# Kernel tuning notes

Measured on AMD Instinct MI355X. Metric: run time of the kernel, lower is better.

Reference implementation:

```python
import jax, jax.numpy as jnp
import numpy as np

N = 50000
E = 1600000
IN, HID, OUT = 32, 64, 64

def setup_inputs() -> dict:
    key = jax.random.key(0)
    ks = jax.random.split(key, 10)
    x1 = jax.random.normal(ks[0], (N, IN), dtype=jnp.float32)
    x2 = jax.random.normal(ks[1], (N, IN), dtype=jnp.float32)
    ei1 = jax.random.randint(ks[2], (2, E), 0, N, dtype=jnp.int64)
    ei2 = jax.random.randint(ks[3], (2, E), 0, N, dtype=jnp.int64)
    s1 = 1.0 / np.sqrt(2 * IN)
    s2 = 1.0 / np.sqrt(2 * HID)
    W1 = jax.random.uniform(ks[4], (2 * IN, HID), jnp.float32, -s1, s1)
    b1 = jax.random.uniform(ks[5], (HID,), jnp.float32, -s1, s1)
    prelu_a = jnp.full((HID,), 0.25, dtype=jnp.float32)  # PReLU per-channel init
    W2 = jax.random.uniform(ks[6], (2 * HID, OUT), jnp.float32, -s2, s2)
    b2 = jax.random.uniform(ks[7], (OUT,), jnp.float32, -s2, s2)
    return {"x1": x1, "edge_index1": ei1, "x2": x2, "edge_index2": ei2,
            "W1": W1, "b1": b1, "prelu_a": prelu_a, "W2": W2, "b2": b2}

def _edge_conv(x, src, dst, W, b, n_nodes):
    # PyG EdgeConv: msg = MLP([x_i, x_j - x_i]), aggr = max over incoming edges
    xi = x[dst]                     # [E, d] target node feats
    xj = x[src]                     # [E, d] source node feats
    msg = jax.nn.relu(jnp.concatenate([xi, xj - xi], axis=-1) @ W + b)  # [E, out]
    agg = jax.ops.segment_max(msg, dst, num_segments=n_nodes)
    return jnp.where(jnp.isfinite(agg), agg, 0.0)  # nodes with no in-edges -> 0

def _prelu(x, a):
    return jnp.where(x >= 0, x, a * x)

def _embed(x, edge_index, W1, b1, prelu_a, W2, b2):
    src, dst = edge_index[0], edge_index[1]
    h = _prelu(_edge_conv(x, src, dst, W1, b1, x.shape[0]), prelu_a)
    return _edge_conv(h, src, dst, W2, b2, x.shape[0])

def reference(x1, edge_index1, x2, edge_index2, W1, b1, prelu_a, W2, b2):
    e1 = _embed(x1, edge_index1, W1, b1, prelu_a, W2, b2)
    e2 = _embed(x2, edge_index2, W1, b1, prelu_a, W2, b2)
    return (e1, e2)
```

## Files before the change

### kernel.cpp

```cpp
#include <hip/hip_runtime.h>
#include <hip/hip_fp16.h>


constexpr int HID   = 64;
constexpr int TILE  = 128;
constexpr int TSH   = 7;
constexpr int HTILE = 64;
constexpr int CAP   = 5120;
constexpr int MAXNB = 512;
constexpr int EPT   = 8;
constexpr int CAPN  = 96;

typedef _Float16 half8 __attribute__((ext_vector_type(8)));
typedef float    f32x4 __attribute__((ext_vector_type(4)));

__device__ __forceinline__ unsigned int pkmax(unsigned int a, unsigned int b) {
    unsigned int d;
    asm("v_pk_max_f16 %0, %1, %2" : "=v"(d) : "v"(a), "v"(b));
    return d;
}
__device__ __forceinline__ unsigned int f2hbits(float f) {
    const __half h = __float2half_rn(f);
    return (unsigned int)*reinterpret_cast<const unsigned short*>(&h);
}
__device__ __forceinline__ float h2f(unsigned int b16) {
    const unsigned short b = (unsigned short)b16;
    __half h;
    *reinterpret_cast<unsigned short*>(&h) = b;
    return __half2float(h);
}

struct G {
    const float* x;
    const int*   src;
    const int*   dst;
    int* bcnt;
    unsigned int* bin;
    float*          u;
    unsigned short* vk;
    float*          out;
};

__global__ __launch_bounds__(256) void prep_w_kernel(
    const float* __restrict__ W1, const float* __restrict__ W2,
    _Float16* __restrict__ Wc1, _Float16* __restrict__ Wc2,
    unsigned short* __restrict__ vkS0, unsigned short* __restrict__ vkS1, int N)
{
    const int i = blockIdx.x * 256 + threadIdx.x;
    if (i < 32 * 64) {
        const int k = i >> 6, c = i & 63;
        const float lo = W1[k * 64 + c], hi = W1[(32 + k) * 64 + c];
        Wc1[k * 128 + c]      = (_Float16)(lo - hi);
        Wc1[k * 128 + 64 + c] = (_Float16)hi;
    }
    const int j = i - 32 * 64;
    if (j >= 0 && j < 64 * 64) {
        const int k = j >> 6, c = j & 63;
        const float lo = W2[k * 64 + c], hi = W2[(64 + k) * 64 + c];
        Wc2[k * 128 + c]      = (_Float16)(lo - hi);
        Wc2[k * 128 + 64 + c] = (_Float16)hi;
    }
    const int q = i - (32 * 64 + 64 * 64);
    if (q >= 0 && q < 2 * HID) {
        if (q < HID) vkS0[(size_t)N * HID + q]       = 0xFC00u;
        else         vkS1[(size_t)N * HID + (q-HID)] = 0xFC00u;
    }
}

__global__ __launch_bounds__(256) void bin_kernel(G g0, G g1, int E, int NB) {
    const G g = blockIdx.y ? g1 : g0;
    __shared__ int lh[MAXNB];
    __shared__ int lb[MAXNB];
    for (int i = threadIdx.x; i < NB; i += 256) lh[i] = 0;
    __syncthreads();

    const int base = blockIdx.x * 256 * EPT;
    unsigned int rec[EPT];
    int bb[EPT];
    #pragma unroll
    for (int k = 0; k < EPT; ++k) {
        const int i = base + k * 256 + threadIdx.x;
        if (i < E) {
            const int d = g.dst[i];
            const int s = g.src[i];
            rec[k] = ((unsigned int)s << TSH) | (unsigned int)(d & (TILE - 1));
            bb[k]  = d >> TSH;
            atomicAdd(&lh[bb[k]], 1);
        } else bb[k] = -1;
    }
    __syncthreads();
    for (int t = threadIdx.x; t < NB; t += 256) {
        const int c = lh[t];
        lb[t] = c ? atomicAdd(&g.bcnt[t], c) : 0;
        lh[t] = 0;
    }
    __syncthreads();
    #pragma unroll
    for (int k = 0; k < EPT; ++k) {
        if (bb[k] >= 0) {
            const int off = atomicAdd(&lh[bb[k]], 1);
            const int pos = lb[bb[k]] + off;
            if (pos < CAP)
                g.bin[(size_t)bb[k] * CAP + pos] = rec[k];
        }
    }
}

template<int K>
__global__ __launch_bounds__(256) void gemm_mfma_kernel(
    G g0, G g1, const _Float16* __restrict__ Wc,
    const float* __restrict__ bias, int N)
{
    const G g = blockIdx.y ? g1 : g0;
    constexpr int KH = K / 32;
    const int lane = threadIdx.x & 63;
    const int m    = lane & 15;
    const int quad = lane >> 4;
    const int wid  = (blockIdx.x * 256 + threadIdx.x) >> 6;
    const int nW   = (gridDim.x * 256) >> 6;

    half8 bf[8][KH];
    #pragma unroll
    for (int t = 0; t < 8; ++t)
        #pragma unroll
        for (int h = 0; h < KH; ++h)
            #pragma unroll
            for (int j = 0; j < 8; ++j)
                bf[t][h][j] = Wc[(h * 32 + quad * 8 + j) * 128 + t * 16 + m];

    float bv[4];
    #pragma unroll
    for (int t = 0; t < 4; ++t) bv[t] = bias[t * 16 + m];

    const float* __restrict__ inp = (K == 32) ? g.x : g.out;
    const int tiles = (N + 15) / 16;

    for (int tile = wid; tile < tiles; tile += nW) {
        const int nbase = tile * 16;
        const int nodeA = min(nbase + m, N - 1);
        const float4* rp = (const float4*)(inp + (size_t)nodeA * K);

        half8 a[KH];
        #pragma unroll
        for (int h = 0; h < KH; ++h) {
            const float4 f0 = rp[h * 8 + quad * 2];
            const float4 f1 = rp[h * 8 + quad * 2 + 1];
            a[h][0] = (_Float16)f0.x; a[h][1] = (_Float16)f0.y;
            a[h][2] = (_Float16)f0.z; a[h][3] = (_Float16)f0.w;
            a[h][4] = (_Float16)f1.x; a[h][5] = (_Float16)f1.y;
            a[h][6] = (_Float16)f1.z; a[h][7] = (_Float16)f1.w;
        }

        f32x4 acc[8];
        #pragma unroll
        for (int t = 0; t < 8; ++t) {
            acc[t] = (f32x4){0.f, 0.f, 0.f, 0.f};
            #pragma unroll
            for (int h = 0; h < KH; ++h)
                acc[t] = __builtin_amdgcn_mfma_f32_16x16x32_f16(
                    a[h], bf[t][h], acc[t], 0, 0, 0);
        }

        #pragma unroll
        for (int r = 0; r < 4; ++r) {
            const int node = nbase + quad * 4 + r;
            if (node < N) {
                float* urow = g.u + (size_t)node * HID;
                #pragma unroll
                for (int t = 0; t < 4; ++t)
                    urow[t * 16 + m] = acc[t][r] + bv[t];
                const unsigned int e0 = f2hbits(acc[4][r]);
                const unsigned int e1 = f2hbits(acc[5][r]);
                const unsigned int e2 = f2hbits(acc[6][r]);
                const unsigned int e3 = f2hbits(acc[7][r]);
                uint2 pack;
                pack.x = (e1 << 16) | e0;
                pack.y = (e3 << 16) | e2;
                ((uint2*)(g.vk + (size_t)node * HID))[m] = pack;
            }
        }
    }
}

__global__ __launch_bounds__(256) void agg_kernel(G g0, G g1, int N, int NB, int two) {
    int idx, gi;
    if (two) {
        const int bid = blockIdx.x;
        const int xcd = bid & 7;
        gi  = xcd >> 2;
        idx = (bid >> 3) * 4 + (xcd & 3);
    } else { gi = 0; idx = blockIdx.x; }
    if (idx >= 2 * NB) return;
    const int b    = idx >> 1;
    const int half = idx & 1;
    const G g = gi ? g1 : g0;

    __shared__ int lcnt[HTILE];
    __shared__ unsigned short lrec[HTILE][CAPN];
    for (int i = threadIdx.x; i < HTILE; i += 256) lcnt[i] = 0;
    __syncthreads();

    const int cnt  = min(g.bcnt[b], CAP);
    const int hsel = half << 6;
    const unsigned int* __restrict__ bp = g.bin + (size_t)b * CAP;
    for (int i = threadIdx.x; i < cnt; i += 256) {
        const unsigned int rec = bp[i];
        const int d = rec & (TILE - 1);
        if ((d & 64) == hsel) {
            const int p = atomicAdd(&lcnt[d & 63], 1);
            if (p < CAPN) lrec[d & 63][p] = (unsigned short)(rec >> TSH);
        }
    }
    __syncthreads();
    for (int t = threadIdx.x; t < HTILE; t += 256) {
        const int c  = min(lcnt[t], CAPN);
        const int cp = (c + 7) & ~7;
        for (int p = c; p < cp; ++p) lrec[t][p] = (unsigned short)N;
        lcnt[t] = cp;
    }
    __syncthreads();

    const int grp = threadIdx.x >> 4;
    const int sub = threadIdx.x & 15;
    const uint2* __restrict__ vk2 = (const uint2*)g.vk;

    #pragma unroll
    for (int i = 0; i < 4; ++i) {
        const int nl = grp + 16 * i;
        const int n  = b * TILE + half * HTILE + nl;
        if (n >= N) continue;
        const int cp = lcnt[nl];

        unsigned int m0 = 0xFC00FC00u, m1 = 0xFC00FC00u;
        for (int j = 0; j < cp; j += 8) {
            const uint4 rq = *(const uint4*)(&lrec[nl][j]);
            unsigned int s[8];
            s[0] = rq.x & 0xFFFFu; s[1] = rq.x >> 16;
            s[2] = rq.y & 0xFFFFu; s[3] = rq.y >> 16;
            s[4] = rq.z & 0xFFFFu; s[5] = rq.z >> 16;
            s[6] = rq.w & 0xFFFFu; s[7] = rq.w >> 16;
            uint2 a[8];
            #pragma unroll
            for (int k = 0; k < 8; ++k) a[k] = vk2[(size_t)s[k] * 16 + sub];
            #pragma unroll
            for (int k = 0; k < 8; ++k) {
                m0 = pkmax(m0, a[k].x);
                m1 = pkmax(m1, a[k].y);
            }
        }

        float mv[4];
        mv[0] = h2f(m0 & 0xFFFFu); mv[1] = h2f(m0 >> 16);
        mv[2] = h2f(m1 & 0xFFFFu); mv[3] = h2f(m1 >> 16);

        const bool has = cp > 0;
        const float* __restrict__ urow = g.u + (size_t)n * HID;
        float* __restrict__ orow = g.out + (size_t)n * HID;
        #pragma unroll
        for (int t = 0; t < 4; ++t)
            orow[sub + 16 * t] =
                has ? fmaxf(urow[sub + 16 * t] + mv[t], 0.f) : 0.f;
    }
}


extern "C" void kernel_launch(void* const* d_in, const int* in_sizes, int n_in,
                              void* d_out, int out_size, void* d_ws, size_t ws_size,
                              hipStream_t stream) {
    const float* x1  = (const float*)d_in[0];
    const int*   ei1 = (const int*)d_in[1];
    const float* x2  = (const float*)d_in[2];
    const int*   ei2 = (const int*)d_in[3];
    const float* W1  = (const float*)d_in[4];
    const float* b1  = (const float*)d_in[5];
    const float* W2  = (const float*)d_in[7];
    const float* b2  = (const float*)d_in[8];

    const int N  = in_sizes[0] / 32;
    const int E  = in_sizes[1] / 2;
    const int NB = (N + TILE - 1) / TILE;
    float* out = (float*)d_out;

    const size_t rowB = (size_t)N * HID * sizeof(float);
    const size_t vkB  = ((size_t)(N + 1) * HID * 2 + 63) & ~(size_t)63;
    const size_t binB = ((size_t)NB * CAP * sizeof(int) + 63) & ~(size_t)63;
    const size_t nbB  = ((size_t)(NB + 2) * sizeof(int) + 63) & ~(size_t)63;
    const size_t wc1B = ((size_t)32 * 128 * 2 + 63) & ~(size_t)63;
    const size_t wc2B = ((size_t)64 * 128 * 2 + 63) & ~(size_t)63;

    const int bBlk = (E + 256 * EPT - 1) / (256 * EPT);
    const int gBlk = 512;
    const int pBlk = (32 * 64 + 64 * 64 + 2 * HID + 255) / 256;
    const int aggBlk2 = ((2 * NB + 3) / 4) * 8;
    const int aggBlk1 = 2 * NB;

    _Float16* wc1 = nullptr;
    _Float16* wc2 = nullptr;

    auto run = [&](G ga, G gb, int ny) {
        hipMemsetAsync(ga.bcnt, 0, (size_t)ny * nbB, stream);
        bin_kernel <<<dim3(bBlk, ny), 256, 0, stream>>>(ga, gb, E, NB);
        gemm_mfma_kernel<32><<<dim3(gBlk, ny), 256, 0, stream>>>(ga, gb, wc1, b1, N);
        if (ny == 2) agg_kernel<<<aggBlk2, 256, 0, stream>>>(ga, gb, N, NB, 1);
        else         agg_kernel<<<aggBlk1, 256, 0, stream>>>(ga, ga, N, NB, 0);
        gemm_mfma_kernel<64><<<dim3(gBlk, ny), 256, 0, stream>>>(ga, gb, wc2, b2, N);
        if (ny == 2) agg_kernel<<<aggBlk2, 256, 0, stream>>>(ga, gb, N, NB, 1);
        else         agg_kernel<<<aggBlk1, 256, 0, stream>>>(ga, ga, N, NB, 0);
    };

    char* ws = (char*)d_ws;
    const size_t needBoth = 2 * rowB + 2 * vkB + 2 * binB + 2 * nbB + wc1B + wc2B;

    if (ws_size >= needBoth) {
        float* u0 = (float*)ws;                  ws += rowB;
        float* u1 = (float*)ws;                  ws += rowB;
        unsigned int* bin0 = (unsigned int*)ws;  ws += binB;
        unsigned int* bin1 = (unsigned int*)ws;  ws += binB;
        unsigned short* vk0 = (unsigned short*)ws;  ws += vkB;
        unsigned short* vk1 = (unsigned short*)ws;  ws += vkB;
        wc1 = (_Float16*)ws;                     ws += wc1B;
        wc2 = (_Float16*)ws;                     ws += wc2B;
        int* bcnt0 = (int*)ws;                   ws += nbB;
        int* bcnt1 = (int*)ws;

        G g0{x1, ei1, ei1 + E, bcnt0, bin0, u0, vk0, out};
        G g1{x2, ei2, ei2 + E, bcnt1, bin1, u1, vk1, out + (size_t)N * HID};
        prep_w_kernel<<<pBlk, 256, 0, stream>>>(W1, W2, wc1, wc2, vk0, vk1, N);
        run(g0, g1, 2);
    } else {
        float* u = (float*)ws;                   ws += rowB;
        unsigned int* bin = (unsigned int*)ws;   ws += binB;
        unsigned short* vk = (unsigned short*)ws;  ws += vkB;
        wc1 = (_Float16*)ws;                     ws += wc1B;
        wc2 = (_Float16*)ws;                     ws += wc2B;
        int* bcnt = (int*)ws;

        prep_w_kernel<<<pBlk, 256, 0, stream>>>(W1, W2, wc1, wc2, vk, vk, N);
        for (int g = 0; g < 2; ++g) {
            const int* ei = g ? ei2 : ei1;
            G gp{g ? x2 : x1, ei, ei + E, bcnt, bin,
                 u, vk, out + (size_t)g * N * HID};
            run(gp, gp, 1);
        }
    }
}
```

Before: 264.3 us.

## Split aggregation by feature half instead of node half, relayout vk rows

Each aggregation block now covers all 128 destination nodes of a bin but only half of the 64 feature channels, instead of half the nodes with all channels. The vk row layout is changed so each feature half sits in a contiguous 64-byte span, and each gather loads one 32-bit word per edge rather than a uint2. The aim is for each block to touch half the vk bytes per gathered row, which can improve L2 locality when paired with the XCD-based block mapping. In exchange, every block reads and bins the whole bin record list, and the shared memory for lrec doubles.

```diff
diff --git a/kernel.cpp b/kernel.cpp
--- a/kernel.cpp
+++ b/kernel.cpp
@@ -5,7 +5,6 @@
 constexpr int HID   = 64;
 constexpr int TILE  = 128;
 constexpr int TSH   = 7;
-constexpr int HTILE = 64;
 constexpr int CAP   = 5120;
 constexpr int MAXNB = 512;
 constexpr int EPT   = 8;
@@ -173,46 +172,41 @@
                 const unsigned int e1 = f2hbits(acc[5][r]);
                 const unsigned int e2 = f2hbits(acc[6][r]);
                 const unsigned int e3 = f2hbits(acc[7][r]);
-                uint2 pack;
-                pack.x = (e1 << 16) | e0;
-                pack.y = (e3 << 16) | e2;
-                ((uint2*)(g.vk + (size_t)node * HID))[m] = pack;
+                unsigned int* vr = (unsigned int*)(g.vk + (size_t)node * HID);
+                vr[m]      = (e1 << 16) | e0;
+                vr[16 + m] = (e3 << 16) | e2;
             }
         }
     }
 }
 
 __global__ __launch_bounds__(256) void agg_kernel(G g0, G g1, int N, int NB, int two) {
-    int idx, gi;
+    int b, h, gi;
     if (two) {
         const int bid = blockIdx.x;
         const int xcd = bid & 7;
-        gi  = xcd >> 2;
-        idx = (bid >> 3) * 4 + (xcd & 3);
-    } else { gi = 0; idx = blockIdx.x; }
-    if (idx >= 2 * NB) return;
-    const int b    = idx >> 1;
-    const int half = idx & 1;
+        gi = xcd >> 2;
+        h  = (xcd >> 1) & 1;
+        b  = (bid >> 3) * 2 + (xcd & 1);
+    } else { gi = 0; h = blockIdx.x & 1; b = blockIdx.x >> 1; }
+    if (b >= NB) return;
     const G g = gi ? g1 : g0;
 
-    __shared__ int lcnt[HTILE];
-    __shared__ unsigned short lrec[HTILE][CAPN];
-    for (int i = threadIdx.x; i < HTILE; i += 256) lcnt[i] = 0;
-    __syncthreads();
-
-    const int cnt  = min(g.bcnt[b], CAP);
-    const int hsel = half << 6;
+    __shared__ int lcnt[TILE];
+    __shared__ unsigned short lrec[TILE][CAPN];
+    for (int i = threadIdx.x; i < TILE; i += 256) lcnt[i] = 0;
+    __syncthreads();
+
+    const int cnt = min(g.bcnt[b], CAP);
     const unsigned int* __restrict__ bp = g.bin + (size_t)b * CAP;
     for (int i = threadIdx.x; i < cnt; i += 256) {
         const unsigned int rec = bp[i];
         const int d = rec & (TILE - 1);
-        if ((d & 64) == hsel) {
-            const int p = atomicAdd(&lcnt[d & 63], 1);
-            if (p < CAPN) lrec[d & 63][p] = (unsigned short)(rec >> TSH);
-        }
-    }
-    __syncthreads();
-    for (int t = threadIdx.x; t < HTILE; t += 256) {
+        const int p = atomicAdd(&lcnt[d], 1);
+        if (p < CAPN) lrec[d][p] = (unsigned short)(rec >> TSH);
+    }
+    __syncthreads();
+    for (int t = threadIdx.x; t < TILE; t += 256) {
         const int c  = min(lcnt[t], CAPN);
         const int cp = (c + 7) & ~7;
         for (int p = c; p < cp; ++p) lrec[t][p] = (unsigned short)N;
@@ -220,18 +214,19 @@
     }
     __syncthreads();
 
-    const int grp = threadIdx.x >> 4;
-    const int sub = threadIdx.x & 15;
-    const uint2* __restrict__ vk2 = (const uint2*)g.vk;
-
-    #pragma unroll
-    for (int i = 0; i < 4; ++i) {
+    const int grp  = threadIdx.x >> 4;
+    const int sub  = threadIdx.x & 15;
+    const int slot = h * 16 + sub;
+    const unsigned int* __restrict__ vkU = (const unsigned int*)g.vk;
+
+    #pragma unroll 2
+    for (int i = 0; i < 8; ++i) {
         const int nl = grp + 16 * i;
-        const int n  = b * TILE + half * HTILE + nl;
+        const int n  = b * TILE + nl;
         if (n >= N) continue;
         const int cp = lcnt[nl];
 
-        unsigned int m0 = 0xFC00FC00u, m1 = 0xFC00FC00u;
+        unsigned int m0 = 0xFC00FC00u;
         for (int j = 0; j < cp; j += 8) {
             const uint4 rq = *(const uint4*)(&lrec[nl][j]);
             unsigned int s[8];
@@ -239,27 +234,19 @@
             s[2] = rq.y & 0xFFFFu; s[3] = rq.y >> 16;
             s[4] = rq.z & 0xFFFFu; s[5] = rq.z >> 16;
             s[6] = rq.w & 0xFFFFu; s[7] = rq.w >> 16;
-            uint2 a[8];
+            unsigned int a[8];
             #pragma unroll
-            for (int k = 0; k < 8; ++k) a[k] = vk2[(size_t)s[k] * 16 + sub];
+            for (int k = 0; k < 8; ++k) a[k] = vkU[(size_t)s[k] * 32 + slot];
             #pragma unroll
-            for (int k = 0; k < 8; ++k) {
-                m0 = pkmax(m0, a[k].x);
-                m1 = pkmax(m1, a[k].y);
-            }
-        }
-
-        float mv[4];
-        mv[0] = h2f(m0 & 0xFFFFu); mv[1] = h2f(m0 >> 16);
-        mv[2] = h2f(m1 & 0xFFFFu); mv[3] = h2f(m1 >> 16);
+            for (int k = 0; k < 8; ++k) m0 = pkmax(m0, a[k]);
+        }
 
         const bool has = cp > 0;
+        const int  cb  = sub + 32 * h;
         const float* __restrict__ urow = g.u + (size_t)n * HID;
         float* __restrict__ orow = g.out + (size_t)n * HID;
-        #pragma unroll
-        for (int t = 0; t < 4; ++t)
-            orow[sub + 16 * t] =
-                has ? fmaxf(urow[sub + 16 * t] + mv[t], 0.f) : 0.f;
+        orow[cb] = has ? fmaxf(urow[cb] + h2f(m0 & 0xFFFFu), 0.f) : 0.f;
+        orow[cb + 16] = has ? fmaxf(urow[cb + 16] + h2f(m0 >> 16), 0.f) : 0.f;
     }
 }
 
@@ -291,7 +278,7 @@
     const int bBlk = (E + 256 * EPT - 1) / (256 * EPT);
     const int gBlk = 512;
     const int pBlk = (32 * 64 + 64 * 64 + 2 * HID + 255) / 256;
-    const int aggBlk2 = ((2 * NB + 3) / 4) * 8;
+    const int aggBlk2 = ((NB + 1) / 2) * 8;
     const int aggBlk1 = 2 * NB;
 
     _Float16* wc1 = nullptr;
```

Result: slower. 324.7 us (+22.9%).
